# Kernel optimization log

Measured on AMD Instinct MI355X. Metric: run time of the kernel, lower is better.

## Reference

```python
import jax, jax.numpy as jnp
import numpy as np

B, L, D = 64, 256, 768
LABELS = 200
REL_OFF = 256  # to_pos[k] = k + 256


def setup_inputs() -> dict:
    key = jax.random.key(0)
    ks = jax.random.split(key, 8)
    return {
        "sequence_output": jax.random.normal(ks[0], (B, L, D), dtype=jnp.float32),
        "pos_embedding": jax.random.normal(ks[1], (2 * REL_OFF + 1, D), dtype=jnp.float32) * 0.02,
        "class_embedding": jax.random.normal(ks[2], (LABELS + 1, D), dtype=jnp.float32) * 0.02,
        "W": jax.random.normal(ks[3], (LABELS, 3 * D), dtype=jnp.float32) * 0.02,
        "b": jnp.zeros((LABELS,), dtype=jnp.float32),
        "head_indexes": jax.random.randint(ks[4], (B, L), 0, L),
        "frame": jax.random.randint(ks[5], (B,), 0, LABELS + 1),
        "pos": jax.random.randint(ks[6], (B,), 0, L),
    }


def reference(sequence_output, pos_embedding, class_embedding, W, b, head_indexes, frame, pos):
    # per-batch gather of token rows: sequence_output[i] = sequence_output[i][head_indexes[i]]
    gathered = jnp.take_along_axis(sequence_output, head_indexes[:, :, None], axis=1)  # [B,L,D]

    j = jnp.arange(sequence_output.shape[1])  # [L]
    rel = j[None, :] - pos[:, None] + REL_OFF  # [B,L] in [0, 512]
    pe = pos_embedding[rel]  # [B,L,D]

    # frame embedding only at j == pos[i], else class_embedding[0]
    fe_hit = class_embedding[frame]  # [B,D]
    is_pos = (j[None, :] == pos[:, None])[:, :, None]  # [B,L,1]
    fe = jnp.where(is_pos, fe_hit[:, None, :], class_embedding[0][None, None, :])  # [B,L,D]

    feat = jnp.concatenate([gathered, pe, fe], axis=-1)  # [B,L,3D]
    # dropout is identity at inference; classifier linear
    return jnp.einsum("blf,cf->blc", feat, W) + b
```

## Files before the change

### kernel.cpp

```cpp
#include <hip/hip_runtime.h>
#include <stdint.h>


typedef __attribute__((ext_vector_type(8))) short short8;
typedef __attribute__((ext_vector_type(4))) float f32x4;
typedef __attribute__((ext_vector_type(16))) float f32x16;

#define AS1 __attribute__((address_space(1)))
#define AS3 __attribute__((address_space(3)))

#define NSEQ_G 1572864
#define NPE_G  49248
#define NCE_G  19296
#define NW32_G 73728
#define SEQB_OFF 0
#define PEB_OFF  12582912
#define CEB_OFF  (PEB_OFF + 393984)
#define WP_OFF   (CEB_OFF + 154368)
#define WS_ELEMS (WP_OFF + 589824)
#define WS_NEED  ((size_t)WS_ELEMS * 2)
#define T32_STRIDE 73728

__device__ __forceinline__ unsigned short f2bf(float f) {
    union { float f; unsigned int u; } v; v.f = f;
    unsigned int u = v.u;
    return (unsigned short)((u + 0x7fffu + ((u >> 16) & 1u)) >> 16);
}

__device__ __forceinline__ short8 pack8(f32x4 a, f32x4 b) {
    short8 r;
    r[0] = (short)f2bf(a.x); r[1] = (short)f2bf(a.y);
    r[2] = (short)f2bf(a.z); r[3] = (short)f2bf(a.w);
    r[4] = (short)f2bf(b.x); r[5] = (short)f2bf(b.y);
    r[6] = (short)f2bf(b.z); r[7] = (short)f2bf(b.w);
    return r;
}

__device__ __forceinline__ void dma16(const unsigned short* g, AS3 unsigned short* l) {
    __builtin_amdgcn_global_load_lds((AS1 const unsigned int*)g,
                                     (AS3 unsigned int*)l, 16, 0, 0);
}

__global__ void prep_kernel(const float* __restrict__ seq,
                            const float* __restrict__ pe,
                            const float* __restrict__ ce,
                            const float* __restrict__ W,
                            unsigned short* __restrict__ ws) {
    int g = blockIdx.x * 256 + threadIdx.x;
    if (g < NSEQ_G) {
        const float* p = seq + (size_t)g * 8;
        *(short8*)(ws + SEQB_OFF + (size_t)g * 8) =
            pack8(*(const f32x4*)p, *(const f32x4*)(p + 4));
        return;
    }
    g -= NSEQ_G;
    if (g < NPE_G) {
        const float* p = pe + (size_t)g * 8;
        *(short8*)(ws + PEB_OFF + (size_t)g * 8) =
            pack8(*(const f32x4*)p, *(const f32x4*)(p + 4));
        return;
    }
    g -= NPE_G;
    if (g < NCE_G) {
        const float* p = ce + (size_t)g * 8;
        *(short8*)(ws + CEB_OFF + (size_t)g * 8) =
            pack8(*(const f32x4*)p, *(const f32x4*)(p + 4));
        return;
    }
    g -= NCE_G;
    if (g < NW32_G) {
        int n  = g & 31;
        int k8 = (g >> 5) % 288;
        int t  = g / (288 * 32);
        int row = t * 32 + n;
        int col = k8 * 8;
        f32x4 a = {0.f, 0.f, 0.f, 0.f}, b = {0.f, 0.f, 0.f, 0.f};
        if (row < 200) {
            const float* p = W + (size_t)row * 2304 + col;
            a = *(const f32x4*)p;
            b = *(const f32x4*)(p + 4);
        }
        *(short8*)(ws + WP_OFF + (size_t)g * 8) = pack8(a, b);
    }
}

__global__ __launch_bounds__(128) void gemm10_kernel(
    const unsigned short* __restrict__ ws,
    const float* __restrict__ bias,
    const int*   __restrict__ head,
    const int*   __restrict__ frame,
    const int*   __restrict__ pos,
    float* __restrict__ out)
{
    __shared__ unsigned short ldsA[4096];
    __shared__ unsigned short ldsB[8192];

    const unsigned short* seqb = ws + SEQB_OFF;
    const unsigned short* peb  = ws + PEB_OFF;
    const unsigned short* ceb  = ws + CEB_OFF;
    const unsigned short* Wp   = ws + WP_OFF;

    const int tid  = threadIdx.x;
    const int wave = tid >> 6;
    const int lane = tid & 63;
    const int n32  = lane & 31;
    const int half = lane >> 5;

    const int mblk = blockIdx.x & 255;
    const int nh   = blockIdx.x >> 8;

    const int i       = mblk >> 2;
    const int pos_i   = pos[i];
    const int frame_i = frame[i];

    const int arow = mblk * 64 + wave * 32 + n32;
    const unsigned short *aSeg[3];
    {
        const int aj   = arow & 255;
        const int ahi  = head[arow];
        const int arel = aj - pos_i + 256;
        const int acls = (aj == pos_i) ? frame_i : 0;
        const int loff = half * 8;
        aSeg[0] = seqb + ((size_t)i * 256 + (size_t)ahi) * 768 + loff;
        aSeg[1] = peb + (size_t)arel * 768 + loff;
        aSeg[2] = ceb + (size_t)acls * 768 + loff;
    }
    AS3 unsigned short* aD = (AS3 unsigned short*)ldsA + wave * 2048 + lane * 8;

    const unsigned short* bSt0 = Wp + (size_t)(nh * 4 + 2 * wave) * T32_STRIDE + lane * 8;
    const unsigned short* bSt1 = bSt0 + T32_STRIDE;
    AS3 unsigned short* bD = (AS3 unsigned short*)ldsB + (2 * wave) * 2048 + lane * 8;

    f32x16 acc[2][2];
#pragma unroll
    for (int ni = 0; ni < 2; ++ni) {
        const int col = nh * 128 + (2 * wave + ni) * 32 + n32;
        const float bv = (col < 200) ? bias[col] : 0.0f;
#pragma unroll
        for (int f = 0; f < 2; ++f)
#pragma unroll
            for (int r = 0; r < 16; ++r) acc[f][ni][r] = bv;
    }

    const int bRd0 = (2 * wave) * 2048 + lane * 8;

#pragma unroll
    for (int sg = 0; sg < 3; ++sg) {
        const unsigned short* aSrc = aSeg[sg];
        for (int cc = 0; cc < 12; ++cc) {
            const int c = sg * 12 + cc;
#pragma unroll
            for (int kb = 0; kb < 4; ++kb)
                dma16(aSrc + cc * 64 + kb * 16, aD + kb * 512);
#pragma unroll
            for (int r = 0; r < 4; ++r) {
                dma16(bSt0 + (size_t)c * 2048 + r * 512, bD + r * 512);
                dma16(bSt1 + (size_t)c * 2048 + r * 512, bD + 2048 + r * 512);
            }
            __syncthreads();
#pragma unroll
            for (int kb = 0; kb < 4; ++kb) {
                short8 a0 = *(const short8*)(ldsA + kb * 512 + lane * 8);
                short8 a1 = *(const short8*)(ldsA + 2048 + kb * 512 + lane * 8);
                short8 b0 = *(const short8*)(ldsB + bRd0 + kb * 512);
                short8 b1 = *(const short8*)(ldsB + bRd0 + 2048 + kb * 512);
                acc[0][0] = __builtin_amdgcn_mfma_f32_32x32x16_bf16(a0, b0, acc[0][0], 0, 0, 0);
                acc[1][0] = __builtin_amdgcn_mfma_f32_32x32x16_bf16(a1, b0, acc[1][0], 0, 0, 0);
                acc[0][1] = __builtin_amdgcn_mfma_f32_32x32x16_bf16(a0, b1, acc[0][1], 0, 0, 0);
                acc[1][1] = __builtin_amdgcn_mfma_f32_32x32x16_bf16(a1, b1, acc[1][1], 0, 0, 0);
            }
            __syncthreads();
        }
    }

#pragma unroll
    for (int f = 0; f < 2; ++f) {
        const int rb = mblk * 64 + f * 32 + 4 * half;
#pragma unroll
        for (int ni = 0; ni < 2; ++ni) {
            const int col = nh * 128 + (2 * wave + ni) * 32 + n32;
            if (col < 200) {
#pragma unroll
                for (int r = 0; r < 16; ++r) {
                    const int row = rb + (r & 3) + 8 * (r >> 2);
                    out[(size_t)row * 200 + col] = acc[f][ni][r];
                }
            }
        }
    }
}

__global__ __launch_bounds__(256) void gemm_fallback(
    const float* __restrict__ seq, const float* __restrict__ pe,
    const float* __restrict__ ce, const float* __restrict__ Wf,
    const float* __restrict__ bias, const int* __restrict__ head,
    const int* __restrict__ frame, const int* __restrict__ pos,
    float* __restrict__ out)
{
    const int tid  = threadIdx.x;
    const int wave = tid >> 6;
    const int lane = tid & 63;
    const int n16  = lane & 15;
    const int quad = lane >> 4;

    const int mrow  = blockIdx.x * 16 + n16;
    const int i     = mrow >> 8;
    const int j     = mrow & 255;
    const int pos_i = pos[i];
    const int hi    = head[mrow];
    const int rel   = j - pos_i + 256;
    const int cls   = (j == pos_i) ? frame[i] : 0;

    const float* segs[3];
    segs[0] = seq + ((size_t)i * 256 + (size_t)hi) * 768 + quad * 8;
    segs[1] = pe + (size_t)rel * 768 + quad * 8;
    segs[2] = ce + (size_t)cls * 768 + quad * 8;

    const int ntl = (wave == 0) ? 4 : 3;
    f32x4 acc[4];
#pragma unroll
    for (int u = 0; u < 4; ++u) {
        const int t = wave + 4 * u;
        const int col = t * 16 + n16;
        const float bv = (t < 13 && col < 200) ? bias[col] : 0.0f;
        acc[u] = (f32x4){bv, bv, bv, bv};
    }

    for (int s = 0; s < 3; ++s) {
        const float* ap = segs[s];
#pragma unroll 2
        for (int kk = 0; kk < 768; kk += 32) {
            short8 afr = pack8(*(const f32x4*)(ap + kk), *(const f32x4*)(ap + kk + 4));
#pragma unroll
            for (int u = 0; u < 4; ++u) {
                if (u < ntl) {
                    const int t = wave + 4 * u;
                    const int row = t * 16 + n16;
                    short8 bfr = {0, 0, 0, 0, 0, 0, 0, 0};
                    if (row < 200) {
                        const float* qp = Wf + (size_t)row * 2304 + s * 768 + kk + quad * 8;
                        bfr = pack8(*(const f32x4*)qp, *(const f32x4*)(qp + 4));
                    }
                    acc[u] = __builtin_amdgcn_mfma_f32_16x16x32_bf16(afr, bfr, acc[u], 0, 0, 0);
                }
            }
        }
    }

    const int rbase = blockIdx.x * 16 + quad * 4;
#pragma unroll
    for (int u = 0; u < 4; ++u) {
        const int t = wave + 4 * u;
        if (t < 13) {
            const int col = t * 16 + n16;
            if (col < 200) {
#pragma unroll
                for (int r = 0; r < 4; ++r)
                    out[(size_t)(rbase + r) * 200 + col] = acc[u][r];
            }
        }
    }
}

extern "C" void kernel_launch(void* const* d_in, const int* in_sizes, int n_in,
                              void* d_out, int out_size, void* d_ws, size_t ws_size,
                              hipStream_t stream) {
    const float* seq  = (const float*)d_in[0];
    const float* pe   = (const float*)d_in[1];
    const float* ce   = (const float*)d_in[2];
    const float* W    = (const float*)d_in[3];
    const float* bias = (const float*)d_in[4];
    const int* head   = (const int*)d_in[5];
    const int* frame  = (const int*)d_in[6];
    const int* pos    = (const int*)d_in[7];
    float* out = (float*)d_out;

    if (d_ws != nullptr && ws_size >= WS_NEED) {
        unsigned short* ws = (unsigned short*)d_ws;
        const int total_g = NSEQ_G + NPE_G + NCE_G + NW32_G;
        prep_kernel<<<(total_g + 255) / 256, 256, 0, stream>>>(seq, pe, ce, W, ws);
        gemm10_kernel<<<512, 128, 0, stream>>>(ws, bias, head, frame, pos, out);
    } else {
        gemm_fallback<<<1024, 256, 0, stream>>>(seq, pe, ce, W, bias, head,
                                                frame, pos, out);
    }
}
```

Baseline: 137.6 us.

## Split GEMM K dimension into three segments with atomic accumulation

Splits the K=2304 reduction into three blocks, one per feature segment (sequence, position, class embedding), tripling the grid from 512 to 1536 blocks. Output is pre-initialized with the bias by a new kernel and each block atomically adds its partial result. This is meant to raise occupancy and parallelism on a GPU with many CUs, since 512 blocks underfill the device. In exchange it adds an extra kernel launch, three times the output writes as atomics, and a non-deterministic summation order.

```diff
diff --git a/kernel.cpp b/kernel.cpp
--- a/kernel.cpp
+++ b/kernel.cpp
@@ -84,9 +84,14 @@
     }
 }
 
-__global__ __launch_bounds__(128) void gemm10_kernel(
+__global__ void init_out_kernel(const float* __restrict__ bias,
+                                float* __restrict__ out) {
+    const int c = threadIdx.x;
+    if (c < 200) out[(size_t)blockIdx.x * 200 + c] = bias[c];
+}
+
+__global__ __launch_bounds__(128) void gemm11_kernel(
     const unsigned short* __restrict__ ws,
-    const float* __restrict__ bias,
     const int*   __restrict__ head,
     const int*   __restrict__ frame,
     const int*   __restrict__ pos,
@@ -95,10 +100,7 @@
     __shared__ unsigned short ldsA[4096];
     __shared__ unsigned short ldsB[8192];
 
-    const unsigned short* seqb = ws + SEQB_OFF;
-    const unsigned short* peb  = ws + PEB_OFF;
-    const unsigned short* ceb  = ws + CEB_OFF;
-    const unsigned short* Wp   = ws + WP_OFF;
+    const unsigned short* Wp = ws + WP_OFF;
 
     const int tid  = threadIdx.x;
     const int wave = tid >> 6;
@@ -106,71 +108,70 @@
     const int n32  = lane & 31;
     const int half = lane >> 5;
 
-    const int mblk = blockIdx.x & 255;
-    const int nh   = blockIdx.x >> 8;
+    const int bx   = blockIdx.x;
+    const int sg   = bx >> 9;
+    const int rr   = bx & 511;
+    const int mblk = rr & 255;
+    const int nh   = rr >> 8;
 
     const int i       = mblk >> 2;
     const int pos_i   = pos[i];
     const int frame_i = frame[i];
 
     const int arow = mblk * 64 + wave * 32 + n32;
-    const unsigned short *aSeg[3];
+    const unsigned short* aSrc;
     {
         const int aj   = arow & 255;
         const int ahi  = head[arow];
         const int arel = aj - pos_i + 256;
         const int acls = (aj == pos_i) ? frame_i : 0;
         const int loff = half * 8;
-        aSeg[0] = seqb + ((size_t)i * 256 + (size_t)ahi) * 768 + loff;
-        aSeg[1] = peb + (size_t)arel * 768 + loff;
-        aSeg[2] = ceb + (size_t)acls * 768 + loff;
+        if (sg == 0)
+            aSrc = ws + SEQB_OFF + ((size_t)i * 256 + (size_t)ahi) * 768 + loff;
+        else if (sg == 1)
+            aSrc = ws + PEB_OFF + (size_t)arel * 768 + loff;
+        else
+            aSrc = ws + CEB_OFF + (size_t)acls * 768 + loff;
     }
     AS3 unsigned short* aD = (AS3 unsigned short*)ldsA + wave * 2048 + lane * 8;
 
-    const unsigned short* bSt0 = Wp + (size_t)(nh * 4 + 2 * wave) * T32_STRIDE + lane * 8;
+    const unsigned short* bSt0 =
+        Wp + (size_t)(nh * 4 + 2 * wave) * T32_STRIDE + (size_t)sg * 24576 + lane * 8;
     const unsigned short* bSt1 = bSt0 + T32_STRIDE;
     AS3 unsigned short* bD = (AS3 unsigned short*)ldsB + (2 * wave) * 2048 + lane * 8;
 
     f32x16 acc[2][2];
 #pragma unroll
-    for (int ni = 0; ni < 2; ++ni) {
-        const int col = nh * 128 + (2 * wave + ni) * 32 + n32;
-        const float bv = (col < 200) ? bias[col] : 0.0f;
-#pragma unroll
-        for (int f = 0; f < 2; ++f)
-#pragma unroll
-            for (int r = 0; r < 16; ++r) acc[f][ni][r] = bv;
-    }
+    for (int f = 0; f < 2; ++f)
+#pragma unroll
+        for (int ni = 0; ni < 2; ++ni)
+#pragma unroll
+            for (int r = 0; r < 16; ++r) acc[f][ni][r] = 0.0f;
 
     const int bRd0 = (2 * wave) * 2048 + lane * 8;
 
-#pragma unroll
-    for (int sg = 0; sg < 3; ++sg) {
-        const unsigned short* aSrc = aSeg[sg];
-        for (int cc = 0; cc < 12; ++cc) {
-            const int c = sg * 12 + cc;
-#pragma unroll
-            for (int kb = 0; kb < 4; ++kb)
-                dma16(aSrc + cc * 64 + kb * 16, aD + kb * 512);
-#pragma unroll
-            for (int r = 0; r < 4; ++r) {
-                dma16(bSt0 + (size_t)c * 2048 + r * 512, bD + r * 512);
-                dma16(bSt1 + (size_t)c * 2048 + r * 512, bD + 2048 + r * 512);
-            }
-            __syncthreads();
-#pragma unroll
-            for (int kb = 0; kb < 4; ++kb) {
-                short8 a0 = *(const short8*)(ldsA + kb * 512 + lane * 8);
-                short8 a1 = *(const short8*)(ldsA + 2048 + kb * 512 + lane * 8);
-                short8 b0 = *(const short8*)(ldsB + bRd0 + kb * 512);
-                short8 b1 = *(const short8*)(ldsB + bRd0 + 2048 + kb * 512);
-                acc[0][0] = __builtin_amdgcn_mfma_f32_32x32x16_bf16(a0, b0, acc[0][0], 0, 0, 0);
-                acc[1][0] = __builtin_amdgcn_mfma_f32_32x32x16_bf16(a1, b0, acc[1][0], 0, 0, 0);
-                acc[0][1] = __builtin_amdgcn_mfma_f32_32x32x16_bf16(a0, b1, acc[0][1], 0, 0, 0);
-                acc[1][1] = __builtin_amdgcn_mfma_f32_32x32x16_bf16(a1, b1, acc[1][1], 0, 0, 0);
-            }
-            __syncthreads();
-        }
+    for (int cc = 0; cc < 12; ++cc) {
+#pragma unroll
+        for (int kb = 0; kb < 4; ++kb)
+            dma16(aSrc + cc * 64 + kb * 16, aD + kb * 512);
+#pragma unroll
+        for (int r = 0; r < 4; ++r) {
+            dma16(bSt0 + (size_t)cc * 2048 + r * 512, bD + r * 512);
+            dma16(bSt1 + (size_t)cc * 2048 + r * 512, bD + 2048 + r * 512);
+        }
+        __syncthreads();
+#pragma unroll
+        for (int kb = 0; kb < 4; ++kb) {
+            short8 a0 = *(const short8*)(ldsA + kb * 512 + lane * 8);
+            short8 a1 = *(const short8*)(ldsA + 2048 + kb * 512 + lane * 8);
+            short8 b0 = *(const short8*)(ldsB + bRd0 + kb * 512);
+            short8 b1 = *(const short8*)(ldsB + bRd0 + 2048 + kb * 512);
+            acc[0][0] = __builtin_amdgcn_mfma_f32_32x32x16_bf16(a0, b0, acc[0][0], 0, 0, 0);
+            acc[1][0] = __builtin_amdgcn_mfma_f32_32x32x16_bf16(a1, b0, acc[1][0], 0, 0, 0);
+            acc[0][1] = __builtin_amdgcn_mfma_f32_32x32x16_bf16(a0, b1, acc[0][1], 0, 0, 0);
+            acc[1][1] = __builtin_amdgcn_mfma_f32_32x32x16_bf16(a1, b1, acc[1][1], 0, 0, 0);
+        }
+        __syncthreads();
     }
 
 #pragma unroll
@@ -183,7 +184,7 @@
 #pragma unroll
                 for (int r = 0; r < 16; ++r) {
                     const int row = rb + (r & 3) + 8 * (r >> 2);
-                    out[(size_t)row * 200 + col] = acc[f][ni][r];
+                    atomicAdd(&out[(size_t)row * 200 + col], acc[f][ni][r]);
                 }
             }
         }
@@ -279,7 +280,8 @@
         unsigned short* ws = (unsigned short*)d_ws;
         const int total_g = NSEQ_G + NPE_G + NCE_G + NW32_G;
         prep_kernel<<<(total_g + 255) / 256, 256, 0, stream>>>(seq, pe, ce, W, ws);
-        gemm10_kernel<<<512, 128, 0, stream>>>(ws, bias, head, frame, pos, out);
+        init_out_kernel<<<16384, 256, 0, stream>>>(bias, out);
+        gemm11_kernel<<<1536, 128, 0, stream>>>(ws, head, frame, pos, out);
     } else {
         gemm_fallback<<<1024, 256, 0, stream>>>(seq, pe, ce, W, bias, head,
                                                 frame, pos, out);
```

Result: slower. 164.9 us (+19.8%).
